# Kernel optimization log

Measured on AMD Instinct MI355X. Metric: run time of the kernel, lower is better.

Reference implementation:

```python
import jax, jax.numpy as jnp
import numpy as np

NUM_HEADS = 32
NUM_KV_HEADS = 8
HEAD_DIM = 128
SCALE = 0.08838834764831845  # 1/sqrt(128)
BATCH = 16
NUM_BLOCKS = 4096
BLOCK_SIZE = 16
BLOCKS_PER_SEQ = 256
MAX_SEQ = BLOCKS_PER_SEQ * BLOCK_SIZE  # 4096


def setup_inputs() -> dict:
    key = jax.random.key(0)
    ks = jax.random.split(key, 8)
    q = jax.random.normal(ks[0], (BATCH, NUM_HEADS, HEAD_DIM), dtype=jnp.float32)
    k = jax.random.normal(ks[1], (BATCH, NUM_KV_HEADS, HEAD_DIM), dtype=jnp.float32)
    v = jax.random.normal(ks[2], (BATCH, NUM_KV_HEADS, HEAD_DIM), dtype=jnp.float32)
    k_cache = jax.random.normal(ks[3], (NUM_BLOCKS, BLOCK_SIZE, NUM_KV_HEADS, HEAD_DIM), dtype=jnp.float32)
    v_cache = jax.random.normal(ks[4], (NUM_BLOCKS, BLOCK_SIZE, NUM_KV_HEADS, HEAD_DIM), dtype=jnp.float32)
    block_tables = jax.random.randint(ks[5], (BATCH, BLOCKS_PER_SEQ), 0, NUM_BLOCKS, dtype=jnp.int32)
    context_lens = jax.random.randint(ks[6], (BATCH,), 1, MAX_SEQ, dtype=jnp.int32)
    slot_mapping = jax.random.randint(ks[7], (BATCH,), 0, NUM_BLOCKS * BLOCK_SIZE, dtype=jnp.int32)
    return {"q": q, "k": k, "v": v, "k_cache": k_cache, "v_cache": v_cache,
            "block_tables": block_tables, "context_lens": context_lens,
            "slot_mapping": slot_mapping}


def reference(q, k, v, k_cache, v_cache, block_tables, context_lens, slot_mapping):
    B = q.shape[0]
    n_rep = NUM_HEADS // NUM_KV_HEADS

    # store_kvcache: scatter new K/V tokens into the flat-slot view of the cache
    kc = k_cache.reshape(-1, NUM_KV_HEADS, HEAD_DIM).at[slot_mapping].set(k)
    vc = v_cache.reshape(-1, NUM_KV_HEADS, HEAD_DIM).at[slot_mapping].set(v)
    kc = kc.reshape(k_cache.shape)
    vc = vc.reshape(v_cache.shape)

    # paged gather: [B, nb, bs, KV, D] -> [B, S, KV, D]
    k_seq = kc[block_tables].reshape(B, -1, NUM_KV_HEADS, HEAD_DIM)
    v_seq = vc[block_tables].reshape(B, -1, NUM_KV_HEADS, HEAD_DIM)
    S = k_seq.shape[1]

    # GQA: group query heads instead of materializing repeat_kv (same math)
    qg = q.reshape(B, NUM_KV_HEADS, n_rep, HEAD_DIM)
    scores = jnp.einsum('bgrd,bsgd->bgrs', qg, k_seq) * SCALE  # [B, KV, n_rep, S]

    valid = jnp.arange(S, dtype=jnp.int32)[None, :] < context_lens[:, None]  # [B, S]
    scores = jnp.where(valid[:, None, None, :], scores, -jnp.inf)
    p = jax.nn.softmax(scores, axis=-1)

    o = jnp.einsum('bgrs,bsgd->bgrd', p, v_seq)  # [B, KV, n_rep, D]
    return o.reshape(B, NUM_HEADS, HEAD_DIM)
```

## Files before the change

### kernel.cpp

```cpp
#include <hip/hip_runtime.h>
#include <math.h>

#define BATCH 16
#define NH 32
#define KVH 8
#define NREP 4
#define HD 128
#define BS 16
#define BPS 256
#define MAXSEQ 4096
#define NSPLIT_MAX 32
#define CH 64
#define KT_STRIDE 33
#define ATT_SCALE 0.08838834764831845f
#define REC (NREP * HD + 2 * NREP)

__global__ __launch_bounds__(256) void kv_scatter(
    const float* __restrict__ k, const float* __restrict__ v,
    const int* __restrict__ slot_mapping,
    float* __restrict__ k_cache, float* __restrict__ v_cache) {
  int b = blockIdx.x;
  int slot = slot_mapping[b];
  size_t base = (size_t)slot * (KVH * HD) + threadIdx.x * 4;
  size_t src = (size_t)b * (KVH * HD) + threadIdx.x * 4;
  *(float4*)(k_cache + base) = *(const float4*)(k + src);
  *(float4*)(v_cache + base) = *(const float4*)(v + src);
}

__global__ __launch_bounds__(256) void attn_decode(
    const float* __restrict__ q,
    const float* __restrict__ k_cache,
    const float* __restrict__ v_cache,
    const int* __restrict__ block_tables,
    const int* __restrict__ context_lens,
    float* __restrict__ part,
    float* __restrict__ out,
    int nsplits) {
  const int split = blockIdx.x;
  const int kvh   = blockIdx.y;
  const int b     = blockIdx.z;
  const int tid   = threadIdx.x;
  const int ctx   = context_lens[b];
  const int span  = MAXSEQ / nsplits;
  const int s_begin = split * span;

  float* rec = part + (((size_t)b * KVH + kvh) * nsplits + split) * REC;

  if (s_begin >= ctx) {
    if (nsplits > 1 && tid < NREP) {
      rec[NREP * HD + tid] = -INFINITY;
      rec[NREP * HD + NREP + tid] = 0.f;
    }
    return;
  }
  const int s_end = min(ctx, s_begin + span);

  __shared__ float4 kt[CH * KT_STRIDE];
  __shared__ float4 sq[NREP * 32];
  __shared__ float  sc[NREP][CH];
  __shared__ int    btab[CH / BS];
  __shared__ float  alpha_sh[NREP], l_sh[NREP];

  const int wave = tid >> 6;
  const int lane = tid & 63;
  const int grp  = tid >> 5;
  const int gl   = tid & 31;

  if (tid < NREP * 32)
    sq[tid] = *(const float4*)(
        q + ((size_t)b * NH + kvh * NREP + (tid >> 5)) * HD + (tid & 31) * 4);

  float m_w = -INFINITY, l_w = 0.f;
  float acc[NREP][4];
#pragma unroll
  for (int h = 0; h < NREP; ++h)
#pragma unroll
    for (int j = 0; j < 4; ++j) acc[h][j] = 0.f;

  const size_t head_off = (size_t)kvh * HD;

  for (int c0 = s_begin; c0 < s_end; c0 += CH) {
    const int n_tok = min(s_end - c0, CH);

    __syncthreads();
    if (tid < CH / BS) btab[tid] = block_tables[b * BPS + (c0 >> 4) + tid];
    __syncthreads();

    {
      const int c = tid & 31;
      int r = tid >> 5;
#pragma unroll
      for (int i = 0; i < CH / 8; ++i, r += 8) {
        int blk = btab[r >> 4];
        kt[r * KT_STRIDE + c] = *(const float4*)(
            k_cache + ((size_t)blk * BS + (r & 15)) * (KVH * HD) + head_off + c * 4);
      }
    }
    __syncthreads();

    {
      const int t = lane;
      const float4* krow = &kt[t * KT_STRIDE];
      const float4* qh = &sq[wave * 32];
      float4 ps = {0.f, 0.f, 0.f, 0.f};
#pragma unroll 8
      for (int c = 0; c < 32; ++c) {
        float4 kk = krow[c];
        float4 qq = qh[c];
        ps.x += kk.x * qq.x;
        ps.y += kk.y * qq.y;
        ps.z += kk.z * qq.z;
        ps.w += kk.w * qq.w;
      }
      const bool valid = t < n_tok;
      float s = (ps.x + ps.y + ps.z + ps.w) * ATT_SCALE;
      float mloc = valid ? s : -INFINITY;
#pragma unroll
      for (int off = 1; off < 64; off <<= 1)
        mloc = fmaxf(mloc, __shfl_xor(mloc, off));
      float m_new = fmaxf(m_w, mloc);
      float e = valid ? __expf(s - m_new) : 0.f;
      float sum = e;
#pragma unroll
      for (int off = 1; off < 64; off <<= 1) sum += __shfl_xor(sum, off);
      float alpha = (m_w == -INFINITY) ? 0.f : __expf(m_w - m_new);
      l_w = l_w * alpha + sum;
      m_w = m_new;
      sc[wave][t] = e;
      if (lane == 0) alpha_sh[wave] = alpha;
    }
    __syncthreads();

    {
      float a0 = alpha_sh[0], a1 = alpha_sh[1], a2 = alpha_sh[2], a3 = alpha_sh[3];
#pragma unroll
      for (int j = 0; j < 4; ++j) {
        acc[0][j] *= a0; acc[1][j] *= a1; acc[2][j] *= a2; acc[3][j] *= a3;
      }
      for (int t = grp; t < n_tok; t += 8) {
        int blk = btab[t >> 4];
        const float4 vv = *(const float4*)(
            v_cache + ((size_t)blk * BS + (t & 15)) * (KVH * HD) + head_off + gl * 4);
#pragma unroll
        for (int h = 0; h < NREP; ++h) {
          float pp = sc[h][t];
          acc[h][0] += pp * vv.x;
          acc[h][1] += pp * vv.y;
          acc[h][2] += pp * vv.z;
          acc[h][3] += pp * vv.w;
        }
      }
    }
  }

  if (lane == 0) {
    l_sh[wave] = l_w;
    if (nsplits > 1) {
      rec[NREP * HD + wave] = m_w;
      rec[NREP * HD + NREP + wave] = l_w;
    }
  }
  float* red = (float*)kt;
#pragma unroll
  for (int h = 0; h < NREP; ++h)
#pragma unroll
    for (int j = 0; j < 4; ++j)
      red[(grp * NREP + h) * HD + gl * 4 + j] = acc[h][j];
  __syncthreads();

  for (int o = tid; o < NREP * HD; o += 256) {
    float s = 0.f;
#pragma unroll
    for (int g = 0; g < 8; ++g) s += red[(g * NREP) * HD + o];
    int h = o >> 7, d = o & 127;
    if (nsplits == 1) {
      out[((size_t)b * NH + kvh * NREP + h) * HD + d] = s / l_sh[h];
    } else {
      rec[o] = s;
    }
  }
}

__global__ __launch_bounds__(256) void attn_combine(
    const float* __restrict__ part, float* __restrict__ out, int nsplits) {
  const int kvh = blockIdx.x;
  const int b   = blockIdx.y;
  const int tid = threadIdx.x;
  const float* base = part + ((size_t)b * KVH + kvh) * nsplits * REC;

  __shared__ float w_sh[NSPLIT_MAX][NREP];
  __shared__ float L_sh[NREP];

  if (tid < NREP) {
    const int h = tid;
    float M = -INFINITY;
    for (int s = 0; s < nsplits; ++s)
      M = fmaxf(M, base[s * REC + NREP * HD + h]);
    float L = 0.f;
    for (int s = 0; s < nsplits; ++s) {
      float m = base[s * REC + NREP * HD + h];
      float l = base[s * REC + NREP * HD + NREP + h];
      float w = (l > 0.f) ? __expf(m - M) : 0.f;
      w_sh[s][h] = w;
      L += l * w;
    }
    L_sh[h] = L;
  }
  __syncthreads();

  for (int o = tid; o < NREP * HD; o += 256) {
    int h = o >> 7, d = o & 127;
    float s = 0.f;
    for (int sp = 0; sp < nsplits; ++sp) {
      float w = w_sh[sp][h];
      if (w > 0.f) s += w * base[sp * REC + o];
    }
    out[((size_t)b * NH + kvh * NREP + h) * HD + d] = s / L_sh[h];
  }
}

extern "C" void kernel_launch(void* const* d_in, const int* in_sizes, int n_in,
                              void* d_out, int out_size, void* d_ws, size_t ws_size,
                              hipStream_t stream) {
  const float* q = (const float*)d_in[0];
  const float* k = (const float*)d_in[1];
  const float* v = (const float*)d_in[2];
  float* k_cache = (float*)d_in[3];
  float* v_cache = (float*)d_in[4];
  const int* block_tables = (const int*)d_in[5];
  const int* context_lens = (const int*)d_in[6];
  const int* slot_mapping = (const int*)d_in[7];
  float* out  = (float*)d_out;
  float* part = (float*)d_ws;

  kv_scatter<<<BATCH, 256, 0, stream>>>(k, v, slot_mapping, k_cache, v_cache);

  int nsplits = NSPLIT_MAX;
  while (nsplits > 1 &&
         (size_t)BATCH * KVH * nsplits * REC * sizeof(float) > ws_size)
    nsplits >>= 1;

  dim3 grid(nsplits, KVH, BATCH);
  attn_decode<<<grid, 256, 0, stream>>>(q, k_cache, v_cache, block_tables,
                                        context_lens, part, out, nsplits);
  if (nsplits > 1)
    attn_combine<<<dim3(KVH, BATCH), 256, 0, stream>>>(part, out, nsplits);
}
```

Measured before the change: 505.7 us.

## Restructure decode attention to one split per wave with register-only online softmax

Each wave now handles one sequence split independently: 16 lanes cover a token's 128-dim head (8 floats each), and 4 token groups per wave carry their own per-lane online softmax state. QK dot products are reduced with DPP row reductions instead of a shared-memory K tile and block-wide barriers, and the four partial states are merged with shuffles at the end. This removes LDS staging and __syncthreads and issues K and V loads together, at the cost of more registers, redundant exp/rescale work per lane, and a hard-coded split count that no longer checks workspace size.

```diff
diff --git a/kernel.cpp b/kernel.cpp
--- a/kernel.cpp
+++ b/kernel.cpp
@@ -9,11 +9,23 @@
 #define BS 16
 #define BPS 256
 #define MAXSEQ 4096
-#define NSPLIT_MAX 32
-#define CH 64
-#define KT_STRIDE 33
+#define NSPLITS 32
+#define SPAN (MAXSEQ / NSPLITS)
 #define ATT_SCALE 0.08838834764831845f
 #define REC (NREP * HD + 2 * NREP)
+
+__device__ __forceinline__ float rowsum16(float x) {
+  int t;
+  t = __builtin_amdgcn_update_dpp(0, __float_as_int(x), 0x121, 0xf, 0xf, true);
+  x += __int_as_float(t);
+  t = __builtin_amdgcn_update_dpp(0, __float_as_int(x), 0x122, 0xf, 0xf, true);
+  x += __int_as_float(t);
+  t = __builtin_amdgcn_update_dpp(0, __float_as_int(x), 0x124, 0xf, 0xf, true);
+  x += __int_as_float(t);
+  t = __builtin_amdgcn_update_dpp(0, __float_as_int(x), 0x128, 0xf, 0xf, true);
+  x += __int_as_float(t);
+  return x;
+}
 
 __global__ __launch_bounds__(256) void kv_scatter(
     const float* __restrict__ k, const float* __restrict__ v,
@@ -27,177 +39,138 @@
   *(float4*)(v_cache + base) = *(const float4*)(v + src);
 }
 
-__global__ __launch_bounds__(256) void attn_decode(
+__global__ __launch_bounds__(256, 4) void attn_decode(
     const float* __restrict__ q,
     const float* __restrict__ k_cache,
     const float* __restrict__ v_cache,
     const int* __restrict__ block_tables,
     const int* __restrict__ context_lens,
-    float* __restrict__ part,
-    float* __restrict__ out,
-    int nsplits) {
-  const int split = blockIdx.x;
-  const int kvh   = blockIdx.y;
-  const int b     = blockIdx.z;
-  const int tid   = threadIdx.x;
-  const int ctx   = context_lens[b];
-  const int span  = MAXSEQ / nsplits;
-  const int s_begin = split * span;
-
-  float* rec = part + (((size_t)b * KVH + kvh) * nsplits + split) * REC;
-
-  if (s_begin >= ctx) {
-    if (nsplits > 1 && tid < NREP) {
-      rec[NREP * HD + tid] = -INFINITY;
-      rec[NREP * HD + NREP + tid] = 0.f;
-    }
-    return;
-  }
-  const int s_end = min(ctx, s_begin + span);
-
-  __shared__ float4 kt[CH * KT_STRIDE];
-  __shared__ float4 sq[NREP * 32];
-  __shared__ float  sc[NREP][CH];
-  __shared__ int    btab[CH / BS];
-  __shared__ float  alpha_sh[NREP], l_sh[NREP];
-
+    float* __restrict__ part) {
+  const int tid  = threadIdx.x;
   const int wave = tid >> 6;
   const int lane = tid & 63;
-  const int grp  = tid >> 5;
-  const int gl   = tid & 31;
-
-  if (tid < NREP * 32)
-    sq[tid] = *(const float4*)(
-        q + ((size_t)b * NH + kvh * NREP + (tid >> 5)) * HD + (tid & 31) * 4);
-
-  float m_w = -INFINITY, l_w = 0.f;
-  float acc[NREP][4];
-#pragma unroll
-  for (int h = 0; h < NREP; ++h)
-#pragma unroll
-    for (int j = 0; j < 4; ++j) acc[h][j] = 0.f;
-
-  const size_t head_off = (size_t)kvh * HD;
-
-  for (int c0 = s_begin; c0 < s_end; c0 += CH) {
-    const int n_tok = min(s_end - c0, CH);
-
-    __syncthreads();
-    if (tid < CH / BS) btab[tid] = block_tables[b * BPS + (c0 >> 4) + tid];
-    __syncthreads();
-
-    {
-      const int c = tid & 31;
-      int r = tid >> 5;
-#pragma unroll
-      for (int i = 0; i < CH / 8; ++i, r += 8) {
-        int blk = btab[r >> 4];
-        kt[r * KT_STRIDE + c] = *(const float4*)(
-            k_cache + ((size_t)blk * BS + (r & 15)) * (KVH * HD) + head_off + c * 4);
+  const int g    = lane >> 4;
+  const int d16  = lane & 15;
+  const int kvh  = blockIdx.y;
+  const int b    = blockIdx.z;
+  const int split = blockIdx.x * 4 + wave;
+  const int ctx  = context_lens[b];
+  const int s_begin = split * SPAN;
+
+  float* rec = part + (((size_t)b * KVH + kvh) * NSPLITS + split) * REC;
+
+  if (s_begin >= ctx) {
+    if (lane < NREP) {
+      rec[NREP * HD + lane] = -INFINITY;
+      rec[NREP * HD + NREP + lane] = 0.f;
+    }
+    return;
+  }
+  const int s_end = min(ctx, s_begin + SPAN);
+  const int nb = (s_end - s_begin + BS - 1) >> 4;
+
+  float4 qa[NREP], qb[NREP];
+  const float* qp = q + ((size_t)b * NH + kvh * NREP) * HD + d16 * 8;
+#pragma unroll
+  for (int h = 0; h < NREP; ++h) {
+    qa[h] = *(const float4*)(qp + h * HD);
+    qb[h] = *(const float4*)(qp + h * HD + 4);
+  }
+
+  float m[NREP], l[NREP], acc[NREP][8];
+#pragma unroll
+  for (int h = 0; h < NREP; ++h) {
+    m[h] = -INFINITY;
+    l[h] = 0.f;
+#pragma unroll
+    for (int j = 0; j < 8; ++j) acc[h][j] = 0.f;
+  }
+
+  const int* bt = block_tables + b * BPS + (s_begin >> 4);
+  const size_t hoff = (size_t)kvh * HD + d16 * 8;
+
+  for (int cb = 0; cb < nb; ++cb) {
+    const int blk = bt[cb];
+    const size_t pbase = (size_t)blk * BS * (KVH * HD) + hoff;
+    const int tbase = s_begin + cb * BS;
+#pragma unroll
+    for (int i = 0; i < 4; ++i) {
+      const int to = i * 4 + g;
+      const float* kp = k_cache + pbase + (size_t)to * (KVH * HD);
+      const float* vp = v_cache + pbase + (size_t)to * (KVH * HD);
+      float4 ka = *(const float4*)kp;
+      float4 kb = *(const float4*)(kp + 4);
+      float4 va = *(const float4*)vp;
+      float4 vb = *(const float4*)(vp + 4);
+      const bool valid = (tbase + to) < s_end;
+#pragma unroll
+      for (int h = 0; h < NREP; ++h) {
+        float s = ka.x * qa[h].x + ka.y * qa[h].y + ka.z * qa[h].z + ka.w * qa[h].w
+                + kb.x * qb[h].x + kb.y * qb[h].y + kb.z * qb[h].z + kb.w * qb[h].w;
+        s = rowsum16(s) * ATT_SCALE;
+        s = valid ? s : -INFINITY;
+        if (s > m[h]) {
+          float alpha = __expf(m[h] - s);
+          l[h] *= alpha;
+#pragma unroll
+          for (int j = 0; j < 8; ++j) acc[h][j] *= alpha;
+          m[h] = s;
+        }
+        float p = valid ? __expf(s - m[h]) : 0.f;
+        l[h] += p;
+        acc[h][0] += p * va.x; acc[h][1] += p * va.y;
+        acc[h][2] += p * va.z; acc[h][3] += p * va.w;
+        acc[h][4] += p * vb.x; acc[h][5] += p * vb.y;
+        acc[h][6] += p * vb.z; acc[h][7] += p * vb.w;
       }
     }
-    __syncthreads();
-
-    {
-      const int t = lane;
-      const float4* krow = &kt[t * KT_STRIDE];
-      const float4* qh = &sq[wave * 32];
-      float4 ps = {0.f, 0.f, 0.f, 0.f};
-#pragma unroll 8
-      for (int c = 0; c < 32; ++c) {
-        float4 kk = krow[c];
-        float4 qq = qh[c];
-        ps.x += kk.x * qq.x;
-        ps.y += kk.y * qq.y;
-        ps.z += kk.z * qq.z;
-        ps.w += kk.w * qq.w;
-      }
-      const bool valid = t < n_tok;
-      float s = (ps.x + ps.y + ps.z + ps.w) * ATT_SCALE;
-      float mloc = valid ? s : -INFINITY;
-#pragma unroll
-      for (int off = 1; off < 64; off <<= 1)
-        mloc = fmaxf(mloc, __shfl_xor(mloc, off));
-      float m_new = fmaxf(m_w, mloc);
-      float e = valid ? __expf(s - m_new) : 0.f;
-      float sum = e;
-#pragma unroll
-      for (int off = 1; off < 64; off <<= 1) sum += __shfl_xor(sum, off);
-      float alpha = (m_w == -INFINITY) ? 0.f : __expf(m_w - m_new);
-      l_w = l_w * alpha + sum;
-      m_w = m_new;
-      sc[wave][t] = e;
-      if (lane == 0) alpha_sh[wave] = alpha;
-    }
-    __syncthreads();
-
-    {
-      float a0 = alpha_sh[0], a1 = alpha_sh[1], a2 = alpha_sh[2], a3 = alpha_sh[3];
-#pragma unroll
-      for (int j = 0; j < 4; ++j) {
-        acc[0][j] *= a0; acc[1][j] *= a1; acc[2][j] *= a2; acc[3][j] *= a3;
-      }
-      for (int t = grp; t < n_tok; t += 8) {
-        int blk = btab[t >> 4];
-        const float4 vv = *(const float4*)(
-            v_cache + ((size_t)blk * BS + (t & 15)) * (KVH * HD) + head_off + gl * 4);
-#pragma unroll
-        for (int h = 0; h < NREP; ++h) {
-          float pp = sc[h][t];
-          acc[h][0] += pp * vv.x;
-          acc[h][1] += pp * vv.y;
-          acc[h][2] += pp * vv.z;
-          acc[h][3] += pp * vv.w;
-        }
-      }
-    }
-  }
-
-  if (lane == 0) {
-    l_sh[wave] = l_w;
-    if (nsplits > 1) {
-      rec[NREP * HD + wave] = m_w;
-      rec[NREP * HD + NREP + wave] = l_w;
-    }
-  }
-  float* red = (float*)kt;
-#pragma unroll
-  for (int h = 0; h < NREP; ++h)
-#pragma unroll
-    for (int j = 0; j < 4; ++j)
-      red[(grp * NREP + h) * HD + gl * 4 + j] = acc[h][j];
-  __syncthreads();
-
-  for (int o = tid; o < NREP * HD; o += 256) {
-    float s = 0.f;
-#pragma unroll
-    for (int g = 0; g < 8; ++g) s += red[(g * NREP) * HD + o];
-    int h = o >> 7, d = o & 127;
-    if (nsplits == 1) {
-      out[((size_t)b * NH + kvh * NREP + h) * HD + d] = s / l_sh[h];
-    } else {
-      rec[o] = s;
+  }
+
+#pragma unroll
+  for (int h = 0; h < NREP; ++h) {
+    float M = m[h];
+    M = fmaxf(M, __shfl_xor(M, 16));
+    M = fmaxf(M, __shfl_xor(M, 32));
+    float w = (m[h] == -INFINITY) ? 0.f : __expf(m[h] - M);
+    float lw = l[h] * w;
+    lw += __shfl_xor(lw, 16);
+    lw += __shfl_xor(lw, 32);
+#pragma unroll
+    for (int j = 0; j < 8; ++j) {
+      float a = acc[h][j] * w;
+      a += __shfl_xor(a, 16);
+      a += __shfl_xor(a, 32);
+      acc[h][j] = a;
+    }
+    if (lane == 0) {
+      rec[NREP * HD + h] = M;
+      rec[NREP * HD + NREP + h] = lw;
+    }
+    if (g == 0) {
+      float* rp = rec + h * HD + d16 * 8;
+      *(float4*)rp = make_float4(acc[h][0], acc[h][1], acc[h][2], acc[h][3]);
+      *(float4*)(rp + 4) = make_float4(acc[h][4], acc[h][5], acc[h][6], acc[h][7]);
     }
   }
 }
 
 __global__ __launch_bounds__(256) void attn_combine(
-    const float* __restrict__ part, float* __restrict__ out, int nsplits) {
+    const float* __restrict__ part, float* __restrict__ out) {
   const int kvh = blockIdx.x;
   const int b   = blockIdx.y;
   const int tid = threadIdx.x;
-  const float* base = part + ((size_t)b * KVH + kvh) * nsplits * REC;
-
-  __shared__ float w_sh[NSPLIT_MAX][NREP];
+  const float* base = part + ((size_t)b * KVH + kvh) * NSPLITS * REC;
+
+  __shared__ float w_sh[NSPLITS][NREP];
   __shared__ float L_sh[NREP];
 
   if (tid < NREP) {
     const int h = tid;
     float M = -INFINITY;
-    for (int s = 0; s < nsplits; ++s)
+    for (int s = 0; s < NSPLITS; ++s)
       M = fmaxf(M, base[s * REC + NREP * HD + h]);
     float L = 0.f;
-    for (int s = 0; s < nsplits; ++s) {
+    for (int s = 0; s < NSPLITS; ++s) {
       float m = base[s * REC + NREP * HD + h];
       float l = base[s * REC + NREP * HD + NREP + h];
       float w = (l > 0.f) ? __expf(m - M) : 0.f;
@@ -211,7 +184,7 @@
   for (int o = tid; o < NREP * HD; o += 256) {
     int h = o >> 7, d = o & 127;
     float s = 0.f;
-    for (int sp = 0; sp < nsplits; ++sp) {
+    for (int sp = 0; sp < NSPLITS; ++sp) {
       float w = w_sh[sp][h];
       if (w > 0.f) s += w * base[sp * REC + o];
     }
@@ -235,14 +208,8 @@
 
   kv_scatter<<<BATCH, 256, 0, stream>>>(k, v, slot_mapping, k_cache, v_cache);
 
-  int nsplits = NSPLIT_MAX;
-  while (nsplits > 1 &&
-         (size_t)BATCH * KVH * nsplits * REC * sizeof(float) > ws_size)
-    nsplits >>= 1;
-
-  dim3 grid(nsplits, KVH, BATCH);
+  dim3 grid(NSPLITS / 4, KVH, BATCH);
   attn_decode<<<grid, 256, 0, stream>>>(q, k_cache, v_cache, block_tables,
-                                        context_lens, part, out, nsplits);
-  if (nsplits > 1)
-    attn_combine<<<dim3(KVH, BATCH), 256, 0, stream>>>(part, out, nsplits);
-}
+                                        context_lens, part);
+  attn_combine<<<dim3(KVH, BATCH), 256, 0, stream>>>(part, out);
+}
```

Measured after the change: 493.1 us. -2.5%, faster.
